# Performance work log

Hardware: AMD Instinct MI355X
Metric: run time of the kernel (lower is better)

Reference implementation:

```python
import jax, jax.numpy as jnp
import numpy as np

NUM_ITEMS, NUM_USERS, H = 100000, 16384, 48
GCN, ATTN, HID, TOW = 128, 128, 256, 256


def setup_inputs() -> dict:
    key = jax.random.key(0)
    ks = jax.random.split(key, 20)
    s = 0.02
    return {
        'item_feat': jax.random.normal(ks[0], (NUM_ITEMS, 2), jnp.float32),
        'gcn_item_emb': jax.random.normal(ks[1], (NUM_ITEMS, GCN), jnp.float32),
        'gcn_user_emb': jax.random.normal(ks[2], (NUM_USERS, GCN), jnp.float32),
        'hist_idx': jax.random.randint(ks[3], (NUM_USERS, H), 0, NUM_ITEMS, jnp.int32),
        'hist_len': jax.random.randint(ks[4], (NUM_USERS,), 0, H, jnp.int32),
        'Wi1': s * jax.random.normal(ks[5], (GCN + 2, HID), jnp.float32),
        'bi1': jnp.zeros((HID,), jnp.float32),
        'Wi2': s * jax.random.normal(ks[6], (HID, TOW), jnp.float32),
        'bi2': jnp.zeros((TOW,), jnp.float32),
        'Wq': s * jax.random.normal(ks[7], (GCN, ATTN), jnp.float32),
        'bq': jnp.zeros((ATTN,), jnp.float32),
        'Wk': s * jax.random.normal(ks[8], (TOW, ATTN), jnp.float32),
        'bk': jnp.zeros((ATTN,), jnp.float32),
        'Wu1': s * jax.random.normal(ks[9], (GCN + TOW, HID), jnp.float32),
        'bu1': jnp.zeros((HID,), jnp.float32),
        'Wu2': s * jax.random.normal(ks[10], (HID, TOW), jnp.float32),
        'bu2': jnp.zeros((TOW,), jnp.float32),
    }


def _l2norm(x):
    # F.normalize(dim=1): divide by L2 norm clamped to 1e-12
    n = jnp.sqrt(jnp.sum(x * x, axis=1, keepdims=True))
    return x / jnp.maximum(n, 1e-12)


def reference(item_feat, gcn_item_emb, gcn_user_emb, hist_idx, hist_len,
              Wi1, bi1, Wi2, bi2, Wq, bq, Wk, bk, Wu1, bu1, Wu2, bu2):
    # encode_items: [N, 130] -> MLP -> normalized [N, TOW]
    xi = jnp.concatenate([item_feat, gcn_item_emb], axis=1)
    h = jax.nn.relu(xi @ Wi1 + bi1)
    item_emb = _l2norm(h @ Wi2 + bi2)

    # encode_users (batched ragged attention with padding mask)
    item_vecs = item_emb[hist_idx]                       # [U, H, TOW]
    q = gcn_user_emb @ Wq + bq                           # [U, ATTN]
    k = item_vecs @ Wk + bk                              # [U, H, ATTN]
    scores = jnp.einsum('ud,uhd->uh', q, k) / jnp.sqrt(jnp.float32(ATTN))
    mask = jnp.arange(H)[None, :] <= hist_len[:, None]   # >= 1 valid per user
    attn = jax.nn.softmax(jnp.where(mask, scores, -1e30), axis=1)
    hist = jnp.einsum('uh,uhd->ud', attn, item_vecs)     # [U, TOW]
    fused = jnp.concatenate([gcn_user_emb, hist], axis=1)  # [U, 384]
    hu = jax.nn.relu(fused @ Wu1 + bu1)
    user_emb = _l2norm(hu @ Wu2 + bu2)
    return user_emb
```

## Files before the change

### kernel.cpp

```cpp
#include <hip/hip_runtime.h>
#include <hip/hip_bf16.h>
#include <hip/hip_fp8.h>
#include <math.h>

#define NITEMS 100000
#define NUSERS 16384
#define HLEN   48
#define GCN    128
#define ATTN_D 128
#define HID    256
#define TOW    256

typedef __attribute__((ext_vector_type(8))) short short8;
typedef __attribute__((ext_vector_type(16))) unsigned char uchar16;
typedef __attribute__((ext_vector_type(4))) float f32x4;
typedef __hip_bfloat16 bf16;

static __device__ __forceinline__ float bfu(unsigned short u) {
  unsigned int x = ((unsigned int)u) << 16;
  float f; __builtin_memcpy(&f, &x, 4); return f;
}
static __device__ __forceinline__ short f2bf(float v) {
  bf16 h = __float2bfloat16(v);
  short s; __builtin_memcpy(&s, &h, 2); return s;
}
static __device__ __forceinline__ unsigned char f2e4m3(float v) {
  __hip_fp8_e4m3 t(v);
  return (unsigned char)t.__x;
}
static __device__ __forceinline__ float e4m3f(unsigned char b) {
  __hip_fp8_e4m3 t;
  t.__x = (__hip_fp8_storage_t)b;
  return (float)t;
}

#define GLDS16(g, l)                                                            \
  __builtin_amdgcn_global_load_lds(                                             \
      (const __attribute__((address_space(1))) unsigned int*)(g),               \
      (__attribute__((address_space(3))) unsigned int*)(l), 16, 0, 0)

__global__ __launch_bounds__(256) void k_prep_w(const float* __restrict__ W,
                                                bf16* __restrict__ out,
                                                int Korig, int KS, int NT, int perm) {
  int tid = blockIdx.x * 256 + threadIdx.x;
  int total = KS * NT * 512;
  if (tid >= total) return;
  int i  = tid & 7;
  int l  = (tid >> 3) & 63;
  int ct = (tid >> 9) % NT;
  int ks = (tid >> 9) / NT;
  int k   = ks * 32 + ((l >> 4) << 3) + i;
  int col = ct * 16 + (l & 15);
  int N = NT * 16;
  int srck = perm ? ((k < 128) ? (k + 2) : (k - 128)) : k;
  float v = (k < Korig) ? W[(size_t)srck * N + col] : 0.f;
  out[tid] = __float2bfloat16(v);
}

__global__ __launch_bounds__(256) void k_prep_w8(const float* __restrict__ W,
                                                 unsigned char* __restrict__ out,
                                                 int KS, int NT) {
  int tid = blockIdx.x * 256 + threadIdx.x;
  int total = KS * NT * 512;
  if (tid >= total) return;
  int i  = tid & 7;
  int l  = (tid >> 3) & 63;
  int ct = (tid >> 9) % NT;
  int ks = (tid >> 9) / NT;
  int k   = ks * 32 + ((l >> 4) << 3) + i;
  int col = ct * 16 + (l & 15);
  out[tid] = f2e4m3(W[(size_t)k * (NT * 16) + col]);
}

__global__ __launch_bounds__(256) void k_prep_user(const float* __restrict__ gcn_user,
                                                   bf16* __restrict__ fused) {
  int tid = blockIdx.x * 256 + threadIdx.x;
  if (tid >= NUSERS * GCN) return;
  int k = tid & 127;
  int u = tid >> 7;
  fused[(size_t)u * (GCN + TOW) + k] = __float2bfloat16(gcn_user[tid]);
}

__global__ __launch_bounds__(256) void k_fold(const float* __restrict__ Wq,
                                              const float* __restrict__ Wk,
                                              const float* __restrict__ bq,
                                              float* __restrict__ out) {
  const float INV_S = 0.08838834764831845f;
  const int t = threadIdx.x;
  const int b = blockIdx.x;
  if (b < 16) {
    __shared__ float wq[8][128];
    for (int s = t; s < 8 * 128; s += 256)
      wq[s >> 7][s & 127] = Wq[(size_t)(b * 8 + (s >> 7)) * ATTN_D + (s & 127)];
    __syncthreads();
    float acc[8] = {0.f, 0.f, 0.f, 0.f, 0.f, 0.f, 0.f, 0.f};
    for (int d = 0; d < 128; ++d) {
      const float wk = Wk[(size_t)t * ATTN_D + d];
      #pragma unroll
      for (int gg = 0; gg < 8; ++gg) acc[gg] = fmaf(wq[gg][d], wk, acc[gg]);
    }
    #pragma unroll
    for (int gg = 0; gg < 8; ++gg)
      out[(size_t)(b * 8 + gg) * TOW + t] = acc[gg] * INV_S;
  } else {
    float a = 0.f;
    for (int d = 0; d < 128; ++d)
      a = fmaf(bq[d], Wk[(size_t)t * ATTN_D + d], a);
    out[(size_t)128 * TOW + t] = a * INV_S;
  }
}

__global__ __launch_bounds__(512, 2) void k_item_g1(
    const float* __restrict__ feat,
    const float* __restrict__ gcn,
    const bf16* __restrict__ Wf,
    const float* __restrict__ bias,
    unsigned char* __restrict__ h_out,
    int ntiles)
{
  __shared__ bf16 bs[5 * 8192];
  const int j = threadIdx.x;
  const int l = j & 63;
  const int w = j >> 6;
  const int r = l & 15, g = l >> 4;
  const int jb = (j & ~63) * 8;

  #pragma unroll
  for (int s = 0; s < 10; ++s)
    GLDS16(Wf + (size_t)s * 4096 + (size_t)j * 8, &bs[s * 4096 + jb]);

  float bj[16];
  #pragma unroll
  for (int ct = 0; ct < 16; ++ct) bj[ct] = bias[ct * 16 + r];

  __syncthreads();

  for (int t = blockIdx.x; t < ntiles; t += gridDim.x) {
    const int R0 = t * 256 + w * 32;
    int row0 = R0 + r;      if (row0 >= NITEMS) row0 = NITEMS - 1;
    int row1 = R0 + 16 + r; if (row1 >= NITEMS) row1 = NITEMS - 1;
    const float* g0 = gcn + (size_t)row0 * GCN;
    const float* g1 = gcn + (size_t)row1 * GCN;

    f32x4 acc[2][16];
    #pragma unroll
    for (int mr = 0; mr < 2; ++mr)
      #pragma unroll
      for (int ct = 0; ct < 16; ++ct) acc[mr][ct] = (f32x4){0.f, 0.f, 0.f, 0.f};

    #pragma unroll
    for (int ks = 0; ks < 5; ++ks) {
      short8 a0, a1;
      if (ks < 4) {
        const float4* p0 = (const float4*)(g0 + ks * 32 + g * 8);
        const float4* p1 = (const float4*)(g1 + ks * 32 + g * 8);
        float4 x0 = p0[0], y0 = p0[1];
        float4 x1 = p1[0], y1 = p1[1];
        a0[0] = f2bf(x0.x); a0[1] = f2bf(x0.y); a0[2] = f2bf(x0.z); a0[3] = f2bf(x0.w);
        a0[4] = f2bf(y0.x); a0[5] = f2bf(y0.y); a0[6] = f2bf(y0.z); a0[7] = f2bf(y0.w);
        a1[0] = f2bf(x1.x); a1[1] = f2bf(x1.y); a1[2] = f2bf(x1.z); a1[3] = f2bf(x1.w);
        a1[4] = f2bf(y1.x); a1[5] = f2bf(y1.y); a1[6] = f2bf(y1.z); a1[7] = f2bf(y1.w);
      } else {
        a0 = (short8){0, 0, 0, 0, 0, 0, 0, 0};
        a1 = (short8){0, 0, 0, 0, 0, 0, 0, 0};
        if (g == 0) {
          a0[0] = f2bf(feat[(size_t)row0 * 2]);
          a0[1] = f2bf(feat[(size_t)row0 * 2 + 1]);
          a1[0] = f2bf(feat[(size_t)row1 * 2]);
          a1[1] = f2bf(feat[(size_t)row1 * 2 + 1]);
        }
      }
      const bf16* wb = bs + (size_t)(ks * 16) * 512 + (size_t)l * 8;
      #pragma unroll
      for (int ct = 0; ct < 16; ++ct) {
        short8 b = *(const short8*)(wb + ct * 512);
        acc[0][ct] = __builtin_amdgcn_mfma_f32_16x16x32_bf16(a0, b, acc[0][ct], 0, 0, 0);
        acc[1][ct] = __builtin_amdgcn_mfma_f32_16x16x32_bf16(a1, b, acc[1][ct], 0, 0, 0);
      }
    }

    #pragma unroll
    for (int mr = 0; mr < 2; ++mr)
      #pragma unroll
      for (int ct = 0; ct < 16; ++ct)
        #pragma unroll
        for (int i = 0; i < 4; ++i)
          h_out[(size_t)(R0 + mr * 16 + g * 4 + i) * 256 + ct * 16 + r] =
              f2e4m3(fmaxf(acc[mr][ct][i] + bj[ct], 0.f));
  }
}

__global__ __launch_bounds__(512, 4) void k_gemm2_f8(
    const unsigned char* __restrict__ A8,
    const unsigned char* __restrict__ Wf8,
    const float* __restrict__ bias,
    unsigned char* __restrict__ Cout,
    int ntiles)
{
  __shared__ unsigned char bs8[8 * 8192];
  const int j = threadIdx.x;
  const int l = j & 63;
  const int w = j >> 6;
  const int r = l & 15, g = l >> 4;
  const int jb = (j & ~63) * 16;

  #pragma unroll
  for (int s = 0; s < 8; ++s)
    GLDS16(Wf8 + (size_t)s * 8192 + (size_t)j * 16, &bs8[s * 8192 + jb]);

  __syncthreads();

  for (int t = blockIdx.x; t < ntiles; t += gridDim.x) {
    const int R0 = t * 128 + w * 16;
    const unsigned char* arow = A8 + (size_t)(R0 + r) * 256 + g * 8;
    const unsigned char* wbase = bs8 + (size_t)l * 8;

    f32x4 acc[16];
    #pragma unroll
    for (int ct = 0; ct < 16; ++ct) acc[ct] = (f32x4){0.f, 0.f, 0.f, 0.f};

    #pragma unroll 1
    for (int ks = 0; ks < 8; ++ks) {
      long a;
      __builtin_memcpy(&a, arow + ks * 32, 8);
      const unsigned char* wb = wbase + (size_t)(ks * 16) * 512;
      #pragma unroll
      for (int ct = 0; ct < 16; ++ct) {
        long b;
        __builtin_memcpy(&b, wb + ct * 512, 8);
        acc[ct] = __builtin_amdgcn_mfma_f32_16x16x32_fp8_fp8(a, b, acc[ct], 0, 0, 0);
      }
    }

    float s[4] = {0.f, 0.f, 0.f, 0.f};
    #pragma unroll
    for (int ct = 0; ct < 16; ++ct) {
      const float bj = bias[ct * 16 + r];
      #pragma unroll
      for (int i = 0; i < 4; ++i) {
        acc[ct][i] += bj;
        s[i] += acc[ct][i] * acc[ct][i];
      }
    }
    #pragma unroll
    for (int off = 1; off < 16; off <<= 1) {
      #pragma unroll
      for (int i = 0; i < 4; ++i) s[i] += __shfl_xor(s[i], off);
    }
    float rn[4];
    #pragma unroll
    for (int i = 0; i < 4; ++i) rn[i] = 1.f / fmaxf(sqrtf(s[i]), 1e-12f);
    #pragma unroll
    for (int ct = 0; ct < 16; ++ct)
      #pragma unroll
      for (int i = 0; i < 4; ++i)
        Cout[(size_t)(R0 + g * 4 + i) * 256 + ct * 16 + r] =
            f2e4m3(acc[ct][i] * rn[i]);
  }
}

template<int KS, int NT, int MODE, int MR>
__global__ __launch_bounds__(256) void k_gemm(
    const bf16* __restrict__ A,
    const bf16* __restrict__ Wf,
    const float* __restrict__ bias,
    void* __restrict__ Cout,
    int Mtiles, int Astride)
{
  static_assert(NT % 4 == 0, "NT must be divisible by 4");
  constexpr int BSZ = NT * 512;
  constexpr int CH  = NT / 4;
  __shared__ bf16 bs[2][BSZ];
  const int j   = threadIdx.x;
  const int l   = j & 63;
  const int wid = j >> 6;
  int tile = blockIdx.x * 4 + wid;
  if (tile >= Mtiles) tile = Mtiles - 1;
  const int N = NT * 16;
  const int r = l & 15, g = l >> 4;

  {
    const short8* src = (const short8*)Wf;
    short8* dst = (short8*)bs[0];
    #pragma unroll
    for (int c = 0; c < CH; ++c) dst[c * 256 + j] = src[c * 256 + j];
  }

  f32x4 acc[MR][NT];
  #pragma unroll
  for (int mr = 0; mr < MR; ++mr)
    #pragma unroll
    for (int ct = 0; ct < NT; ++ct) acc[mr][ct] = (f32x4){0.f, 0.f, 0.f, 0.f};

  const bf16* arow[MR];
  #pragma unroll
  for (int mr = 0; mr < MR; ++mr)
    arow[mr] = A + (size_t)(tile * (16 * MR) + mr * 16 + r) * Astride + g * 8;

  __syncthreads();

  #pragma unroll
  for (int ks = 0; ks < KS; ++ks) {
    const int cur = ks & 1;
    short8 a[MR];
    #pragma unroll
    for (int mr = 0; mr < MR; ++mr) a[mr] = *(const short8*)(arow[mr] + ks * 32);
    short8 st[CH];
    if (ks + 1 < KS) {
      const short8* src = (const short8*)(Wf + (size_t)(ks + 1) * BSZ);
      #pragma unroll
      for (int c = 0; c < CH; ++c) st[c] = src[c * 256 + j];
    }
    const bf16* wb = bs[cur] + (size_t)l * 8;
    #pragma unroll
    for (int ct = 0; ct < NT; ++ct) {
      short8 b = *(const short8*)(wb + ct * 512);
      #pragma unroll
      for (int mr = 0; mr < MR; ++mr)
        acc[mr][ct] = __builtin_amdgcn_mfma_f32_16x16x32_bf16(a[mr], b, acc[mr][ct], 0, 0, 0);
    }
    if (ks + 1 < KS) {
      short8* dst = (short8*)bs[cur ^ 1];
      #pragma unroll
      for (int c = 0; c < CH; ++c) dst[c * 256 + j] = st[c];
    }
    __syncthreads();
  }

  #pragma unroll
  for (int mr = 0; mr < MR; ++mr) {
    #pragma unroll
    for (int ct = 0; ct < NT; ++ct) {
      const float bj = bias[ct * 16 + r];
      #pragma unroll
      for (int i = 0; i < 4; ++i) acc[mr][ct][i] += bj;
    }
  }

  if (MODE == 0 || MODE == 2 || MODE == 4) {
    #pragma unroll
    for (int mr = 0; mr < MR; ++mr)
      #pragma unroll
      for (int ct = 0; ct < NT; ++ct)
        #pragma unroll
        for (int i = 0; i < 4; ++i) {
          float v = acc[mr][ct][i];
          if (MODE == 0) v = fmaxf(v, 0.f);
          size_t off = (size_t)(tile * (16 * MR) + mr * 16 + g * 4 + i) * N + ct * 16 + r;
          if (MODE == 4) ((float*)Cout)[off] = v;
          else           ((bf16*)Cout)[off]  = __float2bfloat16(v);
        }
  } else {
    #pragma unroll
    for (int mr = 0; mr < MR; ++mr) {
      float s[4] = {0.f, 0.f, 0.f, 0.f};
      #pragma unroll
      for (int ct = 0; ct < NT; ++ct)
        #pragma unroll
        for (int i = 0; i < 4; ++i) s[i] += acc[mr][ct][i] * acc[mr][ct][i];
      #pragma unroll
      for (int off = 1; off < 16; off <<= 1) {
        #pragma unroll
        for (int i = 0; i < 4; ++i) s[i] += __shfl_xor(s[i], off);
      }
      float rn[4];
      #pragma unroll
      for (int i = 0; i < 4; ++i) rn[i] = 1.f / fmaxf(sqrtf(s[i]), 1e-12f);
      #pragma unroll
      for (int ct = 0; ct < NT; ++ct)
        #pragma unroll
        for (int i = 0; i < 4; ++i) {
          size_t off = (size_t)(tile * (16 * MR) + mr * 16 + g * 4 + i) * N + ct * 16 + r;
          float v = acc[mr][ct][i] * rn[i];
          if (MODE == 3) ((float*)Cout)[off] = v;
          else           ((bf16*)Cout)[off]  = __float2bfloat16(v);
        }
    }
  }
}

__global__ __launch_bounds__(256) void k_user_attn(
    const float* __restrict__ Qt,
    const int*   __restrict__ hist_idx,
    const int*   __restrict__ hist_len,
    const unsigned char* __restrict__ emb8,
    bf16* __restrict__ fused)
{
  const int u = blockIdx.x;
  const int j = threadIdx.x;
  const int wid = j >> 6, lane = j & 63;
  const int g = lane >> 4, r = lane & 15;
  const int part = wid * 4 + g;
  __shared__ int   idx[HLEN];
  __shared__ float redO[16][TOW + 4];
  __shared__ float redL[16];

  const int nv = hist_len[u] + 1;

  if (j < HLEN) idx[j] = hist_idx[u * HLEN + j];
  const float* qp = Qt + (size_t)u * TOW + r * 16;
  f32x4 q0 = *(const f32x4*)(qp);
  f32x4 q1 = *(const f32x4*)(qp + 4);
  f32x4 q2 = *(const f32x4*)(qp + 8);
  f32x4 q3 = *(const f32x4*)(qp + 12);
  __syncthreads();

  float l = 0.f;
  f32x4 O0 = (f32x4){0.f,0.f,0.f,0.f}, O1 = O0, O2 = O0, O3 = O0;

  for (int h = part; h < nv; h += 16) {
    const uchar16 e = *(const uchar16*)(emb8 + (size_t)idx[h] * TOW + r * 16);
    float ef[16];
    #pragma unroll
    for (int i = 0; i < 16; ++i) ef[i] = e4m3f(e[i]);

    float sc = q0.x*ef[0] + q0.y*ef[1] + q0.z*ef[2] + q0.w*ef[3]
             + q1.x*ef[4] + q1.y*ef[5] + q1.z*ef[6] + q1.w*ef[7]
             + q2.x*ef[8] + q2.y*ef[9] + q2.z*ef[10]+ q2.w*ef[11]
             + q3.x*ef[12]+ q3.y*ef[13]+ q3.z*ef[14]+ q3.w*ef[15];
    #pragma unroll
    for (int off = 1; off < 16; off <<= 1) sc += __shfl_xor(sc, off);
    const float p = __expf(sc);
    l += p;
    O0.x += p*ef[0];  O0.y += p*ef[1];  O0.z += p*ef[2];  O0.w += p*ef[3];
    O1.x += p*ef[4];  O1.y += p*ef[5];  O1.z += p*ef[6];  O1.w += p*ef[7];
    O2.x += p*ef[8];  O2.y += p*ef[9];  O2.z += p*ef[10]; O2.w += p*ef[11];
    O3.x += p*ef[12]; O3.y += p*ef[13]; O3.z += p*ef[14]; O3.w += p*ef[15];
  }

  *(f32x4*)(&redO[part][r * 16])      = O0;
  *(f32x4*)(&redO[part][r * 16 + 4])  = O1;
  *(f32x4*)(&redO[part][r * 16 + 8])  = O2;
  *(f32x4*)(&redO[part][r * 16 + 12]) = O3;
  if (r == 0) redL[part] = l;
  __syncthreads();

  float L = 0.f, val = 0.f;
  #pragma unroll
  for (int w = 0; w < 16; ++w) {
    L   += redL[w];
    val += redO[w][j];
  }
  fused[(size_t)u * (GCN + TOW) + GCN + j] = __float2bfloat16(val / L);
}

extern "C" void kernel_launch(void* const* d_in, const int* in_sizes, int n_in,
                              void* d_out, int out_size, void* d_ws, size_t ws_size,
                              hipStream_t stream) {
  const float* item_feat = (const float*)d_in[0];
  const float* gcn_item  = (const float*)d_in[1];
  const float* gcn_user  = (const float*)d_in[2];
  const int*   hist_idx  = (const int*)d_in[3];
  const int*   hist_len  = (const int*)d_in[4];
  const float* Wi1 = (const float*)d_in[5];
  const float* bi1 = (const float*)d_in[6];
  const float* Wi2 = (const float*)d_in[7];
  const float* bi2 = (const float*)d_in[8];
  const float* Wq  = (const float*)d_in[9];
  const float* bq  = (const float*)d_in[10];
  const float* Wk  = (const float*)d_in[11];
  const float* bk  = (const float*)d_in[12];
  const float* Wu1 = (const float*)d_in[13];
  const float* bu1 = (const float*)d_in[14];
  const float* Wu2 = (const float*)d_in[15];
  const float* bu2 = (const float*)d_in[16];
  (void)bk;

  char* ws = (char*)d_ws;
  bf16*  Wi1p  = (bf16*)(ws + 0);
  unsigned char* Wi2p8 = (unsigned char*)(ws + 81920);
  bf16*  Wu1p  = (bf16*)(ws + 147456);
  bf16*  Wu2p  = (bf16*)(ws + 344064);
  float* Wqkf  = (float*)(ws + 475136);
  bf16*  Wqkp  = (bf16*)(ws + 607232);
  float* Qt    = (float*)(ws + 672768);
  unsigned char* h8   = (unsigned char*)(ws + 17449984);
  unsigned char* emb8 = (unsigned char*)(ws + 43074560);
  bf16*  fusedA   = (bf16*)(ws + 68699136);
  bf16*  hu_buf   = (bf16*)(ws + 81282048);

  k_prep_w<<<160, 256, 0, stream>>>(Wi1, Wi1p, 130, 5, 16, 1);
  k_prep_w8<<<256, 256, 0, stream>>>(Wi2, Wi2p8, 8, 16);
  k_prep_w<<<384, 256, 0, stream>>>(Wu1, Wu1p, 384, 12, 16, 0);
  k_prep_w<<<256, 256, 0, stream>>>(Wu2, Wu2p, 256, 8, 16, 0);
  k_fold<<<17, 256, 0, stream>>>(Wq, Wk, bq, Wqkf);
  k_prep_w<<<128, 256, 0, stream>>>(Wqkf, Wqkp, 128, 4, 16, 0);
  k_prep_user<<<8192, 256, 0, stream>>>(gcn_user, fusedA);

  const int i256 = (NITEMS + 255) / 256;
  const int i128 = (NITEMS + 127) / 128;
  k_item_g1<<<256, 512, 0, stream>>>(item_feat, gcn_item, Wi1p, bi1, h8, i256);
  k_gemm2_f8<<<512, 512, 0, stream>>>(h8, Wi2p8, bi2, emb8, i128);

  const int utiles = NUSERS / 32;
  const int ublk = utiles / 4;
  k_gemm<4, 16, 4, 2><<<ublk, 256, 0, stream>>>(fusedA, Wqkp, Wqkf + 128 * 256, Qt, utiles, 384);
  k_user_attn<<<NUSERS, 256, 0, stream>>>(Qt, hist_idx, hist_len, emb8, fusedA);
  k_gemm<12, 16, 0, 2><<<ublk, 256, 0, stream>>>(fusedA, Wu1p, bu1, hu_buf, utiles, 384);
  k_gemm<8, 16, 3, 2><<<ublk, 256, 0, stream>>>(hu_buf, Wu2p, bu2, (float*)d_out, utiles, 256);
}
```

Measured before the change: 150.1 us.

## Fold item features into epilogue FMAs and halve per-wave rows in item GEMM1

Drops the fifth MFMA K-step that only carried the two raw item features and instead adds them in the epilogue with two FMAs per output, reading fp32 Wi1 rows 0 and 1 staged in shared memory. Each wave now handles 16 rows instead of 32, which halves the accumulator registers. LDS use drops from 80 KB to 64 KB plus 2 KB, launch bounds go to 4 blocks per SM and the grid doubles to 512 blocks over 128-row tiles. The gain is higher occupancy and less wasted MFMA work. The cost is less reuse of each B fragment per LDS load and an unroll-1 K loop that may expose load latency.

```diff
diff --git a/kernel.cpp b/kernel.cpp
--- a/kernel.cpp
+++ b/kernel.cpp
@@ -110,15 +110,17 @@
   }
 }
 
-__global__ __launch_bounds__(512, 2) void k_item_g1(
+__global__ __launch_bounds__(512, 4) void k_item_g1(
     const float* __restrict__ feat,
     const float* __restrict__ gcn,
     const bf16* __restrict__ Wf,
+    const float* __restrict__ Wi1raw,
     const float* __restrict__ bias,
     unsigned char* __restrict__ h_out,
     int ntiles)
 {
-  __shared__ bf16 bs[5 * 8192];
+  __shared__ bf16  bs[4 * 8192];
+  __shared__ float wfeat[512];
   const int j = threadIdx.x;
   const int l = j & 63;
   const int w = j >> 6;
@@ -126,8 +128,9 @@
   const int jb = (j & ~63) * 8;
 
   #pragma unroll
-  for (int s = 0; s < 10; ++s)
+  for (int s = 0; s < 8; ++s)
     GLDS16(Wf + (size_t)s * 4096 + (size_t)j * 8, &bs[s * 4096 + jb]);
+  wfeat[j] = Wi1raw[j];
 
   float bj[16];
   #pragma unroll
@@ -136,57 +139,49 @@
   __syncthreads();
 
   for (int t = blockIdx.x; t < ntiles; t += gridDim.x) {
-    const int R0 = t * 256 + w * 32;
-    int row0 = R0 + r;      if (row0 >= NITEMS) row0 = NITEMS - 1;
-    int row1 = R0 + 16 + r; if (row1 >= NITEMS) row1 = NITEMS - 1;
-    const float* g0 = gcn + (size_t)row0 * GCN;
-    const float* g1 = gcn + (size_t)row1 * GCN;
-
-    f32x4 acc[2][16];
-    #pragma unroll
-    for (int mr = 0; mr < 2; ++mr)
-      #pragma unroll
-      for (int ct = 0; ct < 16; ++ct) acc[mr][ct] = (f32x4){0.f, 0.f, 0.f, 0.f};
-
-    #pragma unroll
-    for (int ks = 0; ks < 5; ++ks) {
-      short8 a0, a1;
-      if (ks < 4) {
-        const float4* p0 = (const float4*)(g0 + ks * 32 + g * 8);
-        const float4* p1 = (const float4*)(g1 + ks * 32 + g * 8);
-        float4 x0 = p0[0], y0 = p0[1];
-        float4 x1 = p1[0], y1 = p1[1];
-        a0[0] = f2bf(x0.x); a0[1] = f2bf(x0.y); a0[2] = f2bf(x0.z); a0[3] = f2bf(x0.w);
-        a0[4] = f2bf(y0.x); a0[5] = f2bf(y0.y); a0[6] = f2bf(y0.z); a0[7] = f2bf(y0.w);
-        a1[0] = f2bf(x1.x); a1[1] = f2bf(x1.y); a1[2] = f2bf(x1.z); a1[3] = f2bf(x1.w);
-        a1[4] = f2bf(y1.x); a1[5] = f2bf(y1.y); a1[6] = f2bf(y1.z); a1[7] = f2bf(y1.w);
-      } else {
-        a0 = (short8){0, 0, 0, 0, 0, 0, 0, 0};
-        a1 = (short8){0, 0, 0, 0, 0, 0, 0, 0};
-        if (g == 0) {
-          a0[0] = f2bf(feat[(size_t)row0 * 2]);
-          a0[1] = f2bf(feat[(size_t)row0 * 2 + 1]);
-          a1[0] = f2bf(feat[(size_t)row1 * 2]);
-          a1[1] = f2bf(feat[(size_t)row1 * 2 + 1]);
-        }
-      }
+    const int R0 = t * 128 + w * 16;
+    int arow = R0 + r; if (arow >= NITEMS) arow = NITEMS - 1;
+    const float* grow = gcn + (size_t)arow * GCN;
+
+    f32x4 acc[16];
+    #pragma unroll
+    for (int ct = 0; ct < 16; ++ct) acc[ct] = (f32x4){0.f, 0.f, 0.f, 0.f};
+
+    #pragma unroll 1
+    for (int ks = 0; ks < 4; ++ks) {
+      const float4* p = (const float4*)(grow + ks * 32 + g * 8);
+      float4 x = p[0], y = p[1];
+      short8 a;
+      a[0] = f2bf(x.x); a[1] = f2bf(x.y); a[2] = f2bf(x.z); a[3] = f2bf(x.w);
+      a[4] = f2bf(y.x); a[5] = f2bf(y.y); a[6] = f2bf(y.z); a[7] = f2bf(y.w);
       const bf16* wb = bs + (size_t)(ks * 16) * 512 + (size_t)l * 8;
       #pragma unroll
       for (int ct = 0; ct < 16; ++ct) {
         short8 b = *(const short8*)(wb + ct * 512);
-        acc[0][ct] = __builtin_amdgcn_mfma_f32_16x16x32_bf16(a0, b, acc[0][ct], 0, 0, 0);
-        acc[1][ct] = __builtin_amdgcn_mfma_f32_16x16x32_bf16(a1, b, acc[1][ct], 0, 0, 0);
+        acc[ct] = __builtin_amdgcn_mfma_f32_16x16x32_bf16(a, b, acc[ct], 0, 0, 0);
       }
     }
 
-    #pragma unroll
-    for (int mr = 0; mr < 2; ++mr)
-      #pragma unroll
-      for (int ct = 0; ct < 16; ++ct)
-        #pragma unroll
-        for (int i = 0; i < 4; ++i)
-          h_out[(size_t)(R0 + mr * 16 + g * 4 + i) * 256 + ct * 16 + r] =
-              f2e4m3(fmaxf(acc[mr][ct][i] + bj[ct], 0.f));
+    float f0[4], f1[4];
+    #pragma unroll
+    for (int i = 0; i < 4; ++i) {
+      int orow = R0 + g * 4 + i; if (orow >= NITEMS) orow = NITEMS - 1;
+      float2 fv = *(const float2*)(feat + (size_t)orow * 2);
+      f0[i] = fv.x; f1[i] = fv.y;
+    }
+    #pragma unroll
+    for (int ct = 0; ct < 16; ++ct) {
+      const float w0 = wfeat[ct * 16 + r];
+      const float w1 = wfeat[256 + ct * 16 + r];
+      #pragma unroll
+      for (int i = 0; i < 4; ++i) {
+        float v = acc[ct][i] + bj[ct];
+        v = fmaf(f0[i], w0, v);
+        v = fmaf(f1[i], w1, v);
+        h_out[(size_t)(R0 + g * 4 + i) * 256 + ct * 16 + r] =
+            f2e4m3(fmaxf(v, 0.f));
+      }
+    }
   }
 }
 
@@ -487,9 +482,8 @@
   k_prep_w<<<128, 256, 0, stream>>>(Wqkf, Wqkp, 128, 4, 16, 0);
   k_prep_user<<<8192, 256, 0, stream>>>(gcn_user, fusedA);
 
-  const int i256 = (NITEMS + 255) / 256;
   const int i128 = (NITEMS + 127) / 128;
-  k_item_g1<<<256, 512, 0, stream>>>(item_feat, gcn_item, Wi1p, bi1, h8, i256);
+  k_item_g1<<<512, 512, 0, stream>>>(item_feat, gcn_item, Wi1p, Wi1, bi1, h8, i128);
   k_gemm2_f8<<<512, 512, 0, stream>>>(h8, Wi2p8, bi2, emb8, i128);
 
   const int utiles = NUSERS / 32;
```

Result: no change. 148.7 us (-1.0%).
